# Kernel tuning notes

Hardware: AMD Instinct MI355X
Metric: run time of the kernel (lower is better)

## Reference

```python
import jax, jax.numpy as jnp
import numpy as np

N = 8192
E = 262144
IN_DIM, HID, LAT = 256, 256, 128


def _sage_conv(x, src, dst, W_l, b_l, W_r, n_nodes):
    # PyG SAGEConv (mean aggr): out = lin_l(mean_{j in N(i)} x_j) + lin_r(x_i)
    agg = jax.ops.segment_sum(x[src], dst, num_segments=n_nodes)          # [N, F]
    cnt = jax.ops.segment_sum(jnp.ones((src.shape[0],), x.dtype), dst,
                              num_segments=n_nodes)                       # [N]
    mean = agg / jnp.maximum(cnt, 1.0)[:, None]
    return mean @ W_l + b_l + x @ W_r


def setup_inputs() -> dict:
    key = jax.random.key(0)
    ks = jax.random.split(key, 10)
    s = lambda fin: 1.0 / np.sqrt(fin)
    u = lambda k, shape, fin: jax.random.uniform(k, shape, jnp.float32, -s(fin), s(fin))
    inp = {
        "x": jax.random.normal(ks[0], (N, IN_DIM), jnp.float32),
        "edge_index": jax.random.randint(ks[1], (2, E), 0, N, jnp.int64),
        # conv1: in -> hid
        "W_l1": u(ks[2], (IN_DIM, HID), IN_DIM), "b_l1": u(ks[3], (HID,), IN_DIM),
        "W_r1": u(ks[4], (IN_DIM, HID), IN_DIM),
        # conv2 (mu): hid -> lat
        "W_l2": u(ks[5], (HID, LAT), HID), "b_l2": u(ks[6], (LAT,), HID),
        "W_r2": u(ks[7], (HID, LAT), HID),
        # conv3 (logvar): hid -> lat
        "W_l3": u(ks[8], (HID, LAT), HID), "b_l3": jnp.zeros((LAT,), jnp.float32),
        "W_r3": u(ks[9], (HID, LAT), HID),
    }
    return inp


def reference(x, edge_index, W_l1, b_l1, W_r1, W_l2, b_l2, W_r2, W_l3, b_l3, W_r3):
    src, dst = edge_index[0], edge_index[1]
    h = jax.nn.relu(_sage_conv(x, src, dst, W_l1, b_l1, W_r1, N))
    mu = _sage_conv(h, src, dst, W_l2, b_l2, W_r2, N)
    logvar = _sage_conv(h, src, dst, W_l3, b_l3, W_r3, N)
    # reparameterize
    std = jnp.exp(0.5 * logvar)
    eps = jax.random.normal(jax.random.key(42), std.shape, std.dtype)
    z = mu + eps * std
    # inner-product decode on L2-normalized z
    norm_z = z / (jnp.linalg.norm(z, axis=1, keepdims=True) + 1e-8)
    recon_x = norm_z @ norm_z.T                                           # [N, N]
    return recon_x, mu, logvar, z
```

## Files before the change

### kernel.cpp

```cpp
#include <hip/hip_runtime.h>
#include <hip/hip_bf16.h>

#define NN 8192
#define EE 262144
#define IND 256
#define HIDD 256
#define LATD 128
#define CAP 128

typedef __attribute__((ext_vector_type(8))) short bf16x8;
typedef __attribute__((ext_vector_type(4))) float f32x4;

__device__ __forceinline__ unsigned short bf16u(float f) {
    __hip_bfloat16 h = __float2bfloat16(f);
    return *reinterpret_cast<unsigned short*>(&h);
}

__global__ __launch_bounds__(256) void prep_k(
        const float* __restrict__ x, __hip_bfloat16* __restrict__ x_b,
        const float* __restrict__ Wl1, const float* __restrict__ Wr1,
        const float* __restrict__ Wl2, const float* __restrict__ Wr2,
        const float* __restrict__ Wl3, const float* __restrict__ Wr3,
        __hip_bfloat16* __restrict__ Wl1T, __hip_bfloat16* __restrict__ Wr1T,
        __hip_bfloat16* __restrict__ Wl2T, __hip_bfloat16* __restrict__ Wr2T,
        __hip_bfloat16* __restrict__ Wl3T, __hip_bfloat16* __restrict__ Wr3T,
        int* __restrict__ cur) {
    int gid = blockIdx.x * 256 + threadIdx.x;
    if (gid < NN) cur[gid] = 0;
    if (gid < 524288) {
        f32x4 v = reinterpret_cast<const f32x4*>(x)[gid];
        uint2 o;
        o.x = (unsigned)bf16u(v[0]) | ((unsigned)bf16u(v[1]) << 16);
        o.y = (unsigned)bf16u(v[2]) | ((unsigned)bf16u(v[3]) << 16);
        reinterpret_cast<uint2*>(x_b)[gid] = o;
    } else {
        int g2 = gid - 524288;
        if (g2 < 131072) {
            int i = g2 & 65535;
            const float* W = (g2 < 65536) ? Wl1 : Wr1;
            __hip_bfloat16* Wt = (g2 < 65536) ? Wl1T : Wr1T;
            int k = i >> 8, n = i & 255;
            Wt[n * 256 + k] = __float2bfloat16(W[i]);
        } else {
            int g3 = g2 - 131072;
            int w = g3 >> 15, i = g3 & 32767;
            const float* Ws[4] = {Wl2, Wr2, Wl3, Wr3};
            __hip_bfloat16* Wts[4] = {Wl2T, Wr2T, Wl3T, Wr3T};
            int k = i >> 7, n = i & 127;
            Wts[w][n * 256 + k] = __float2bfloat16(Ws[w][i]);
        }
    }
}

__global__ void fill_adj_k(const int* __restrict__ ei, int* __restrict__ cur,
                           int* __restrict__ adj) {
    int e = blockIdx.x * 256 + threadIdx.x;
    if (e < EE) {
        int d = ei[EE + e];
        int p = atomicAdd(&cur[d], 1);
        adj[(d << 7) + p] = ei[e];
    }
}

__global__ __launch_bounds__(256) void agg_mean2_k(
        const __hip_bfloat16* __restrict__ in, const int* __restrict__ adj,
        const int* __restrict__ deg_a, __hip_bfloat16* __restrict__ out) {
    int node = blockIdx.x * 2 + (threadIdx.x >> 7);
    int dp = threadIdx.x & 127;
    const unsigned* inu = (const unsigned*)in;
    int deg = deg_a[node];
    int s = node << 7;
    int e = s + deg;
    float a0 = 0.f, a1 = 0.f;
    int j = s;
    for (; j + 4 <= e; j += 4) {
        int n0 = adj[j], n1 = adj[j + 1], n2 = adj[j + 2], n3 = adj[j + 3];
        unsigned u0 = inu[(size_t)n0 * 128 + dp];
        unsigned u1 = inu[(size_t)n1 * 128 + dp];
        unsigned u2 = inu[(size_t)n2 * 128 + dp];
        unsigned u3 = inu[(size_t)n3 * 128 + dp];
        a0 += __uint_as_float(u0 << 16);
        a1 += __uint_as_float(u0 & 0xffff0000u);
        a0 += __uint_as_float(u1 << 16);
        a1 += __uint_as_float(u1 & 0xffff0000u);
        a0 += __uint_as_float(u2 << 16);
        a1 += __uint_as_float(u2 & 0xffff0000u);
        a0 += __uint_as_float(u3 << 16);
        a1 += __uint_as_float(u3 & 0xffff0000u);
    }
    for (; j < e; ++j) {
        unsigned u = inu[(size_t)adj[j] * 128 + dp];
        a0 += __uint_as_float(u << 16);
        a1 += __uint_as_float(u & 0xffff0000u);
    }
    float w = 1.0f / (float)max(deg, 1);
    unsigned o = (unsigned)bf16u(a0 * w) | ((unsigned)bf16u(a1 * w) << 16);
    ((unsigned*)out)[(size_t)node * 128 + dp] = o;
}

__global__ __launch_bounds__(256) void conv1_k(
        const __hip_bfloat16* __restrict__ A1, const __hip_bfloat16* __restrict__ Bt1,
        const __hip_bfloat16* __restrict__ A2, const __hip_bfloat16* __restrict__ Bt2,
        const float* __restrict__ bias, __hip_bfloat16* __restrict__ outB) {
    int tid = threadIdx.x;
    int wid = tid >> 6, lane = tid & 63;
    int wm = wid >> 1, wn = wid & 1;
    int row0 = blockIdx.x * 128 + wm * 64;
    int col0 = blockIdx.y * 128 + wn * 64;
    int lrow = lane & 15;
    int lk = (lane >> 4) * 8;

    f32x4 acc[4][4] = {};

#pragma unroll
    for (int p = 0; p < 2; ++p) {
        const __hip_bfloat16* A = (p == 0) ? A1 : A2;
        const __hip_bfloat16* Bt = (p == 0) ? Bt1 : Bt2;
        for (int ks = 0; ks < IND; ks += 32) {
            bf16x8 a[4], b[4];
#pragma unroll
            for (int i = 0; i < 4; ++i)
                a[i] = *reinterpret_cast<const bf16x8*>(
                    A + (size_t)(row0 + i * 16 + lrow) * IND + ks + lk);
#pragma unroll
            for (int i = 0; i < 4; ++i)
                b[i] = *reinterpret_cast<const bf16x8*>(
                    Bt + (size_t)(col0 + i * 16 + lrow) * IND + ks + lk);
#pragma unroll
            for (int mi = 0; mi < 4; ++mi)
#pragma unroll
                for (int ni = 0; ni < 4; ++ni)
                    acc[mi][ni] = __builtin_amdgcn_mfma_f32_16x16x32_bf16(
                        a[mi], b[ni], acc[mi][ni], 0, 0, 0);
        }
    }

    int crow = (lane >> 4) * 4;
    int ccol = lane & 15;
#pragma unroll
    for (int mi = 0; mi < 4; ++mi)
#pragma unroll
        for (int ni = 0; ni < 4; ++ni) {
            int col = col0 + ni * 16 + ccol;
            float badd = bias[col];
#pragma unroll
            for (int j = 0; j < 4; ++j) {
                int row = row0 + mi * 16 + crow + j;
                float v = fmaxf(acc[mi][ni][j] + badd, 0.f);
                outB[(size_t)row * HIDD + col] = __float2bfloat16(v);
            }
        }
}

__global__ __launch_bounds__(256) void conv23_k(
        const __hip_bfloat16* __restrict__ meanh, const __hip_bfloat16* __restrict__ h_b,
        const __hip_bfloat16* __restrict__ Wl2T, const __hip_bfloat16* __restrict__ Wr2T,
        const float* __restrict__ bl2,
        const __hip_bfloat16* __restrict__ Wl3T, const __hip_bfloat16* __restrict__ Wr3T,
        const float* __restrict__ bl3,
        float* __restrict__ muF, __hip_bfloat16* __restrict__ muB,
        float* __restrict__ lvF, __hip_bfloat16* __restrict__ lvB) {
    bool is3 = blockIdx.y != 0;
    const __hip_bfloat16* WlT = is3 ? Wl3T : Wl2T;
    const __hip_bfloat16* WrT = is3 ? Wr3T : Wr2T;
    const float* bias = is3 ? bl3 : bl2;
    float* oF = is3 ? lvF : muF;
    __hip_bfloat16* oB = is3 ? lvB : muB;

    int tid = threadIdx.x;
    int wid = tid >> 6, lane = tid & 63;
    int wm = wid >> 1, wn = wid & 1;
    int row0 = blockIdx.x * 128 + wm * 64;
    int col0 = wn * 64;
    int lrow = lane & 15;
    int lk = (lane >> 4) * 8;

    f32x4 acc[4][4] = {};

#pragma unroll
    for (int p = 0; p < 2; ++p) {
        const __hip_bfloat16* A = (p == 0) ? meanh : h_b;
        const __hip_bfloat16* Bt = (p == 0) ? WlT : WrT;
        for (int ks = 0; ks < HIDD; ks += 32) {
            bf16x8 a[4], b[4];
#pragma unroll
            for (int i = 0; i < 4; ++i)
                a[i] = *reinterpret_cast<const bf16x8*>(
                    A + (size_t)(row0 + i * 16 + lrow) * HIDD + ks + lk);
#pragma unroll
            for (int i = 0; i < 4; ++i)
                b[i] = *reinterpret_cast<const bf16x8*>(
                    Bt + (size_t)(col0 + i * 16 + lrow) * HIDD + ks + lk);
#pragma unroll
            for (int mi = 0; mi < 4; ++mi)
#pragma unroll
                for (int ni = 0; ni < 4; ++ni)
                    acc[mi][ni] = __builtin_amdgcn_mfma_f32_16x16x32_bf16(
                        a[mi], b[ni], acc[mi][ni], 0, 0, 0);
        }
    }

    int crow = (lane >> 4) * 4;
    int ccol = lane & 15;
#pragma unroll
    for (int mi = 0; mi < 4; ++mi)
#pragma unroll
        for (int ni = 0; ni < 4; ++ni) {
            int col = col0 + ni * 16 + ccol;
            float badd = bias[col];
#pragma unroll
            for (int j = 0; j < 4; ++j) {
                int row = row0 + mi * 16 + crow + j;
                float v = acc[mi][ni][j] + badd;
                size_t idx = (size_t)row * LATD + col;
                oF[idx] = v;
                oB[idx] = __float2bfloat16(v);
            }
        }
}

__device__ __forceinline__ unsigned rotl32(unsigned x, int r) {
    return (x << r) | (x >> (32 - r));
}

#define TF_ROUND(r)        \
    {                      \
        x0 += x1;          \
        x1 = rotl32(x1, r);\
        x1 ^= x0;          \
    }

__device__ __forceinline__ float tf_normal(unsigned i) {
    const unsigned ks0 = 0u, ks1 = 42u, ks2 = 0u ^ 42u ^ 0x1BD11BDAu;
    unsigned x0 = 0u + ks0;
    unsigned x1 = i + ks1;
    TF_ROUND(13) TF_ROUND(15) TF_ROUND(26) TF_ROUND(6)
    x0 += ks1; x1 += ks2 + 1u;
    TF_ROUND(17) TF_ROUND(29) TF_ROUND(16) TF_ROUND(24)
    x0 += ks2; x1 += ks0 + 2u;
    TF_ROUND(13) TF_ROUND(15) TF_ROUND(26) TF_ROUND(6)
    x0 += ks0; x1 += ks1 + 3u;
    TF_ROUND(17) TF_ROUND(29) TF_ROUND(16) TF_ROUND(24)
    x0 += ks1; x1 += ks2 + 4u;
    TF_ROUND(13) TF_ROUND(15) TF_ROUND(26) TF_ROUND(6)
    x0 += ks2; x1 += ks0 + 5u;
    unsigned bits = x0 ^ x1;
    float f = __uint_as_float((bits >> 9) | 0x3f800000u) - 1.0f;
    const float lo = -0.99999994f;
    float u = fmaxf(f * 2.0f + lo, lo);
    return 1.41421356f * erfinvf(u);
}

__global__ void reparam_norm_k(const __hip_bfloat16* __restrict__ mu_b,
                               const __hip_bfloat16* __restrict__ lv_b,
                               float* __restrict__ z_out, __hip_bfloat16* __restrict__ nz) {
    int row = blockIdx.x;
    int t = threadIdx.x;
    size_t b = (size_t)row * LATD;
    int c0 = t, c1 = t + 64;
    float m0 = __bfloat162float(mu_b[b + c0]);
    float m1 = __bfloat162float(mu_b[b + c1]);
    float s0 = expf(0.5f * __bfloat162float(lv_b[b + c0]));
    float s1 = expf(0.5f * __bfloat162float(lv_b[b + c1]));
    float z0 = m0 + tf_normal((unsigned)(b + c0)) * s0;
    float z1 = m1 + tf_normal((unsigned)(b + c1)) * s1;
    float s = z0 * z0 + z1 * z1;
#pragma unroll
    for (int o = 32; o; o >>= 1) s += __shfl_xor(s, o);
    float inv = 1.0f / (sqrtf(s) + 1e-8f);
    z_out[b + c0] = z0;
    z_out[b + c1] = z1;
    nz[b + c0] = __float2bfloat16(z0 * inv);
    nz[b + c1] = __float2bfloat16(z1 * inv);
}

__global__ __launch_bounds__(256) void recon_k(const __hip_bfloat16* __restrict__ nz,
                                               float* __restrict__ out) {
    __shared__ float lds[128][132];
    int tid = threadIdx.x;
    int wid = tid >> 6, lane = tid & 63;
    int wm = wid >> 1, wn = wid & 1;
    int row0 = blockIdx.x * 128 + wm * 64;
    int col0 = blockIdx.y * 128 + wn * 64;
    int lrow = lane & 15;
    int lk = (lane >> 4) * 8;

    f32x4 acc[4][4] = {};

    for (int ks = 0; ks < LATD; ks += 32) {
        bf16x8 a[4], b[4];
#pragma unroll
        for (int i = 0; i < 4; ++i)
            a[i] = *reinterpret_cast<const bf16x8*>(
                nz + (size_t)(row0 + i * 16 + lrow) * LATD + ks + lk);
#pragma unroll
        for (int i = 0; i < 4; ++i)
            b[i] = *reinterpret_cast<const bf16x8*>(
                nz + (size_t)(col0 + i * 16 + lrow) * LATD + ks + lk);
#pragma unroll
        for (int mi = 0; mi < 4; ++mi)
#pragma unroll
            for (int ni = 0; ni < 4; ++ni)
                acc[mi][ni] = __builtin_amdgcn_mfma_f32_16x16x32_bf16(
                    a[mi], b[ni], acc[mi][ni], 0, 0, 0);
    }

    int crow = (lane >> 4) * 4;
    int ccol = lane & 15;
#pragma unroll
    for (int mi = 0; mi < 4; ++mi)
#pragma unroll
        for (int ni = 0; ni < 4; ++ni) {
            int cl = wn * 64 + ni * 16 + ccol;
            int rb = wm * 64 + mi * 16 + crow;
#pragma unroll
            for (int j = 0; j < 4; ++j) lds[rb + j][cl] = acc[mi][ni][j];
        }
    __syncthreads();

    int r = tid >> 5, c4 = tid & 31;
    size_t base = (size_t)(blockIdx.x * 128) * NN + blockIdx.y * 128;
#pragma unroll
    for (int it = 0; it < 16; ++it) {
        int rr = it * 8 + r;
        f32x4 v = *reinterpret_cast<const f32x4*>(&lds[rr][c4 * 4]);
        __builtin_nontemporal_store(
            v, reinterpret_cast<f32x4*>(&out[base + (size_t)rr * NN + c4 * 4]));
    }
}

extern "C" void kernel_launch(void* const* d_in, const int* in_sizes, int n_in,
                              void* d_out, int out_size, void* d_ws, size_t ws_size,
                              hipStream_t stream) {
    const float* x = (const float*)d_in[0];
    const int* ei = (const int*)d_in[1];
    const float* Wl1 = (const float*)d_in[2];
    const float* bl1 = (const float*)d_in[3];
    const float* Wr1 = (const float*)d_in[4];
    const float* Wl2 = (const float*)d_in[5];
    const float* bl2 = (const float*)d_in[6];
    const float* Wr2 = (const float*)d_in[7];
    const float* Wl3 = (const float*)d_in[8];
    const float* bl3 = (const float*)d_in[9];
    const float* Wr3 = (const float*)d_in[10];

    float* out = (float*)d_out;
    char* ws = (char*)d_ws;

    const size_t MU_OFF = (size_t)NN * NN;
    const size_t LV_OFF = MU_OFF + (size_t)NN * LATD;
    const size_t Z_OFF = LV_OFF + (size_t)NN * LATD;

    int* cur = (int*)(ws + 0);
    int* adj = (int*)(ws + 32768);
    __hip_bfloat16* Wl1T = (__hip_bfloat16*)(ws + 4227072);
    __hip_bfloat16* Wr1T = (__hip_bfloat16*)(ws + 4358144);
    __hip_bfloat16* Wl2T = (__hip_bfloat16*)(ws + 4489216);
    __hip_bfloat16* Wr2T = (__hip_bfloat16*)(ws + 4554752);
    __hip_bfloat16* Wl3T = (__hip_bfloat16*)(ws + 4620288);
    __hip_bfloat16* Wr3T = (__hip_bfloat16*)(ws + 4685824);
    __hip_bfloat16* x_b = (__hip_bfloat16*)(ws + 4751360);
    __hip_bfloat16* meanx = (__hip_bfloat16*)(ws + 8945664);
    __hip_bfloat16* mu_b = (__hip_bfloat16*)(ws + 8945664);
    __hip_bfloat16* lv_b = (__hip_bfloat16*)(ws + 11042816);
    __hip_bfloat16* h_b = (__hip_bfloat16*)(ws + 13139968);
    __hip_bfloat16* meanh = (__hip_bfloat16*)(ws + 17334272);
    __hip_bfloat16* nz = (__hip_bfloat16*)(ws + 21528576);

    prep_k<<<3072, 256, 0, stream>>>(x, x_b, Wl1, Wr1, Wl2, Wr2, Wl3, Wr3,
                                     Wl1T, Wr1T, Wl2T, Wr2T, Wl3T, Wr3T, cur);
    fill_adj_k<<<EE / 256, 256, 0, stream>>>(ei, cur, adj);

    agg_mean2_k<<<NN / 2, 256, 0, stream>>>(x_b, adj, cur, meanx);
    conv1_k<<<dim3(NN / 128, HIDD / 128), 256, 0, stream>>>(meanx, Wl1T, x_b, Wr1T, bl1,
                                                            h_b);

    agg_mean2_k<<<NN / 2, 256, 0, stream>>>(h_b, adj, cur, meanh);
    conv23_k<<<dim3(NN / 128, 2), 256, 0, stream>>>(
        meanh, h_b, Wl2T, Wr2T, bl2, Wl3T, Wr3T, bl3,
        out + MU_OFF, mu_b, out + LV_OFF, lv_b);
    reparam_norm_k<<<NN, 64, 0, stream>>>(mu_b, lv_b, out + Z_OFF, nz);

    recon_k<<<dim3(NN / 128, NN / 128), 256, 0, stream>>>(nz, out);
}
```

Before: 189.1 us.

## Fuse mu/logvar convolutions with reparameterization and row normalization

Merges the conv2/conv3 GEMM kernel and the reparam/normalize kernel into one kernel where each block computes both mu and logvar tiles for 128 rows. It then samples z in registers and reduces row norms through shared-memory atomics. This removes a launch and the bf16 mu/logvar intermediate round-trip through global memory. In exchange, the grid is halved to 64 blocks, each doing double MFMA work with doubled accumulator registers, so parallelism and occupancy drop.

```diff
diff --git a/kernel.cpp b/kernel.cpp
--- a/kernel.cpp
+++ b/kernel.cpp
@@ -152,73 +152,6 @@
         }
 }
 
-__global__ __launch_bounds__(256) void conv23_k(
-        const __hip_bfloat16* __restrict__ meanh, const __hip_bfloat16* __restrict__ h_b,
-        const __hip_bfloat16* __restrict__ Wl2T, const __hip_bfloat16* __restrict__ Wr2T,
-        const float* __restrict__ bl2,
-        const __hip_bfloat16* __restrict__ Wl3T, const __hip_bfloat16* __restrict__ Wr3T,
-        const float* __restrict__ bl3,
-        float* __restrict__ muF, __hip_bfloat16* __restrict__ muB,
-        float* __restrict__ lvF, __hip_bfloat16* __restrict__ lvB) {
-    bool is3 = blockIdx.y != 0;
-    const __hip_bfloat16* WlT = is3 ? Wl3T : Wl2T;
-    const __hip_bfloat16* WrT = is3 ? Wr3T : Wr2T;
-    const float* bias = is3 ? bl3 : bl2;
-    float* oF = is3 ? lvF : muF;
-    __hip_bfloat16* oB = is3 ? lvB : muB;
-
-    int tid = threadIdx.x;
-    int wid = tid >> 6, lane = tid & 63;
-    int wm = wid >> 1, wn = wid & 1;
-    int row0 = blockIdx.x * 128 + wm * 64;
-    int col0 = wn * 64;
-    int lrow = lane & 15;
-    int lk = (lane >> 4) * 8;
-
-    f32x4 acc[4][4] = {};
-
-#pragma unroll
-    for (int p = 0; p < 2; ++p) {
-        const __hip_bfloat16* A = (p == 0) ? meanh : h_b;
-        const __hip_bfloat16* Bt = (p == 0) ? WlT : WrT;
-        for (int ks = 0; ks < HIDD; ks += 32) {
-            bf16x8 a[4], b[4];
-#pragma unroll
-            for (int i = 0; i < 4; ++i)
-                a[i] = *reinterpret_cast<const bf16x8*>(
-                    A + (size_t)(row0 + i * 16 + lrow) * HIDD + ks + lk);
-#pragma unroll
-            for (int i = 0; i < 4; ++i)
-                b[i] = *reinterpret_cast<const bf16x8*>(
-                    Bt + (size_t)(col0 + i * 16 + lrow) * HIDD + ks + lk);
-#pragma unroll
-            for (int mi = 0; mi < 4; ++mi)
-#pragma unroll
-                for (int ni = 0; ni < 4; ++ni)
-                    acc[mi][ni] = __builtin_amdgcn_mfma_f32_16x16x32_bf16(
-                        a[mi], b[ni], acc[mi][ni], 0, 0, 0);
-        }
-    }
-
-    int crow = (lane >> 4) * 4;
-    int ccol = lane & 15;
-#pragma unroll
-    for (int mi = 0; mi < 4; ++mi)
-#pragma unroll
-        for (int ni = 0; ni < 4; ++ni) {
-            int col = col0 + ni * 16 + ccol;
-            float badd = bias[col];
-#pragma unroll
-            for (int j = 0; j < 4; ++j) {
-                int row = row0 + mi * 16 + crow + j;
-                float v = acc[mi][ni][j] + badd;
-                size_t idx = (size_t)row * LATD + col;
-                oF[idx] = v;
-                oB[idx] = __float2bfloat16(v);
-            }
-        }
-}
-
 __device__ __forceinline__ unsigned rotl32(unsigned x, int r) {
     return (x << r) | (x >> (32 - r));
 }
@@ -251,27 +184,97 @@
     return 1.41421356f * erfinvf(u);
 }
 
-__global__ void reparam_norm_k(const __hip_bfloat16* __restrict__ mu_b,
-                               const __hip_bfloat16* __restrict__ lv_b,
-                               float* __restrict__ z_out, __hip_bfloat16* __restrict__ nz) {
-    int row = blockIdx.x;
-    int t = threadIdx.x;
-    size_t b = (size_t)row * LATD;
-    int c0 = t, c1 = t + 64;
-    float m0 = __bfloat162float(mu_b[b + c0]);
-    float m1 = __bfloat162float(mu_b[b + c1]);
-    float s0 = expf(0.5f * __bfloat162float(lv_b[b + c0]));
-    float s1 = expf(0.5f * __bfloat162float(lv_b[b + c1]));
-    float z0 = m0 + tf_normal((unsigned)(b + c0)) * s0;
-    float z1 = m1 + tf_normal((unsigned)(b + c1)) * s1;
-    float s = z0 * z0 + z1 * z1;
-#pragma unroll
-    for (int o = 32; o; o >>= 1) s += __shfl_xor(s, o);
-    float inv = 1.0f / (sqrtf(s) + 1e-8f);
-    z_out[b + c0] = z0;
-    z_out[b + c1] = z1;
-    nz[b + c0] = __float2bfloat16(z0 * inv);
-    nz[b + c1] = __float2bfloat16(z1 * inv);
+__global__ __launch_bounds__(256) void conv23rep_k(
+        const __hip_bfloat16* __restrict__ meanh, const __hip_bfloat16* __restrict__ h_b,
+        const __hip_bfloat16* __restrict__ Wl2T, const __hip_bfloat16* __restrict__ Wr2T,
+        const float* __restrict__ bl2,
+        const __hip_bfloat16* __restrict__ Wl3T, const __hip_bfloat16* __restrict__ Wr3T,
+        const float* __restrict__ bl3,
+        float* __restrict__ muF, float* __restrict__ lvF,
+        float* __restrict__ zF, __hip_bfloat16* __restrict__ nz) {
+    __shared__ float rowsum[128];
+    int tid = threadIdx.x;
+    int wid = tid >> 6, lane = tid & 63;
+    int wm = wid >> 1, wn = wid & 1;
+    int row0 = blockIdx.x * 128 + wm * 64;
+    int col0 = wn * 64;
+    int lrow = lane & 15;
+    int lk = (lane >> 4) * 8;
+
+    f32x4 accM[4][4] = {}, accL[4][4] = {};
+
+#pragma unroll
+    for (int p = 0; p < 2; ++p) {
+        const __hip_bfloat16* A = (p == 0) ? meanh : h_b;
+        const __hip_bfloat16* BtM = (p == 0) ? Wl2T : Wr2T;
+        const __hip_bfloat16* BtL = (p == 0) ? Wl3T : Wr3T;
+        for (int ks = 0; ks < HIDD; ks += 32) {
+            bf16x8 a[4], bM[4], bL[4];
+#pragma unroll
+            for (int i = 0; i < 4; ++i)
+                a[i] = *reinterpret_cast<const bf16x8*>(
+                    A + (size_t)(row0 + i * 16 + lrow) * HIDD + ks + lk);
+#pragma unroll
+            for (int i = 0; i < 4; ++i) {
+                bM[i] = *reinterpret_cast<const bf16x8*>(
+                    BtM + (size_t)(col0 + i * 16 + lrow) * HIDD + ks + lk);
+                bL[i] = *reinterpret_cast<const bf16x8*>(
+                    BtL + (size_t)(col0 + i * 16 + lrow) * HIDD + ks + lk);
+            }
+#pragma unroll
+            for (int mi = 0; mi < 4; ++mi)
+#pragma unroll
+                for (int ni = 0; ni < 4; ++ni) {
+                    accM[mi][ni] = __builtin_amdgcn_mfma_f32_16x16x32_bf16(
+                        a[mi], bM[ni], accM[mi][ni], 0, 0, 0);
+                    accL[mi][ni] = __builtin_amdgcn_mfma_f32_16x16x32_bf16(
+                        a[mi], bL[ni], accL[mi][ni], 0, 0, 0);
+                }
+        }
+    }
+
+    int crow = (lane >> 4) * 4;
+    int ccol = lane & 15;
+    if (tid < 128) rowsum[tid] = 0.f;
+    __syncthreads();
+
+#pragma unroll
+    for (int mi = 0; mi < 4; ++mi)
+#pragma unroll
+        for (int j = 0; j < 4; ++j) {
+            float ps = 0.f;
+            int lrowz = wm * 64 + mi * 16 + crow + j;
+            int grow = blockIdx.x * 128 + lrowz;
+#pragma unroll
+            for (int ni = 0; ni < 4; ++ni) {
+                int col = col0 + ni * 16 + ccol;
+                size_t idx = (size_t)grow * LATD + col;
+                float m = accM[mi][ni][j] + bl2[col];
+                float l = accL[mi][ni][j] + bl3[col];
+                muF[idx] = m;
+                lvF[idx] = l;
+                float zz = m + tf_normal((unsigned)idx) * expf(0.5f * l);
+                zF[idx] = zz;
+                accM[mi][ni][j] = zz;
+                ps += zz * zz;
+            }
+            atomicAdd(&rowsum[lrowz], ps);
+        }
+    __syncthreads();
+
+#pragma unroll
+    for (int mi = 0; mi < 4; ++mi)
+#pragma unroll
+        for (int j = 0; j < 4; ++j) {
+            int lrowz = wm * 64 + mi * 16 + crow + j;
+            int grow = blockIdx.x * 128 + lrowz;
+            float inv = 1.0f / (sqrtf(rowsum[lrowz]) + 1e-8f);
+#pragma unroll
+            for (int ni = 0; ni < 4; ++ni) {
+                int col = col0 + ni * 16 + ccol;
+                nz[(size_t)grow * LATD + col] = __float2bfloat16(accM[mi][ni][j] * inv);
+            }
+        }
 }
 
 __global__ __launch_bounds__(256) void recon_k(const __hip_bfloat16* __restrict__ nz,
@@ -361,8 +364,6 @@
     __hip_bfloat16* Wr3T = (__hip_bfloat16*)(ws + 4685824);
     __hip_bfloat16* x_b = (__hip_bfloat16*)(ws + 4751360);
     __hip_bfloat16* meanx = (__hip_bfloat16*)(ws + 8945664);
-    __hip_bfloat16* mu_b = (__hip_bfloat16*)(ws + 8945664);
-    __hip_bfloat16* lv_b = (__hip_bfloat16*)(ws + 11042816);
     __hip_bfloat16* h_b = (__hip_bfloat16*)(ws + 13139968);
     __hip_bfloat16* meanh = (__hip_bfloat16*)(ws + 17334272);
     __hip_bfloat16* nz = (__hip_bfloat16*)(ws + 21528576);
@@ -376,10 +377,9 @@
                                                             h_b);
 
     agg_mean2_k<<<NN / 2, 256, 0, stream>>>(h_b, adj, cur, meanh);
-    conv23_k<<<dim3(NN / 128, 2), 256, 0, stream>>>(
-        meanh, h_b, Wl2T, Wr2T, bl2, Wl3T, Wr3T, bl3,
-        out + MU_OFF, mu_b, out + LV_OFF, lv_b);
-    reparam_norm_k<<<NN, 64, 0, stream>>>(mu_b, lv_b, out + Z_OFF, nz);
+    conv23rep_k<<<NN / 128, 256, 0, stream>>>(meanh, h_b, Wl2T, Wr2T, bl2, Wl3T, Wr3T,
+                                              bl3, out + MU_OFF, out + LV_OFF,
+                                              out + Z_OFF, nz);
 
     recon_k<<<dim3(NN / 128, NN / 128), 256, 0, stream>>>(nz, out);
 }
```

New measurement: 221.2 us. 17.0% more time.
